# Optimization experiments

Hardware: AMD Instinct MI355X
Metric: run time of the kernel (lower is better)

The kernel has to match this reference:

```python
import jax, jax.numpy as jnp
import numpy as np

HEADS = 16
DIM_HEAD = 64
MAX_FREQ = 256.0  # lucidrains RotaryEmbedding(freqs_for='pixel', max_freq=256)


def axial_freqs(H, W, dim_head):
    # per-axis rotary dim = dim_head // 2 (RotaryEmbedding(dim=head_dim//2))
    d = dim_head // 2
    base = jnp.linspace(1.0, MAX_FREQ / 2.0, d // 2) * jnp.pi  # (d/2,)

    def axis(n):
        pos = jnp.linspace(-1.0, 1.0, n)              # pixel positions
        f = pos[:, None] * base                        # (n, d/2)
        return jnp.repeat(f, 2, axis=-1)               # (n, d) interleaved pairs

    fh = jnp.broadcast_to(axis(H)[:, None, :], (H, W, d))
    fw = jnp.broadcast_to(axis(W)[None, :, :], (H, W, d))
    return jnp.concatenate([fh, fw], axis=-1)          # (H, W, dim_head)


def apply_rope(t, freqs):
    # t: (B,T,H,W,h,d); freqs: (H,W,d)
    f = freqs[:, :, None, :]                           # broadcast over heads
    x = t.reshape(t.shape[:-1] + (t.shape[-1] // 2, 2))
    x1, x2 = x[..., 0], x[..., 1]
    rot = jnp.stack([-x2, x1], axis=-1).reshape(t.shape)  # rotate_half (interleaved)
    return t * jnp.cos(f) + rot * jnp.sin(f)


def setup_inputs() -> dict:
    key = jax.random.key(0)
    k1, k2, k3 = jax.random.split(key, 3)
    B, T, H, W, D = 1, 8, 32, 32, 1024
    inner = HEADS * DIM_HEAD
    x = jax.random.normal(k1, (B, T, H, W, D), dtype=jnp.float32)
    Wqkv = jax.random.normal(k2, (D, 3 * inner), dtype=jnp.float32) * 0.02
    Wout = jax.random.normal(k3, (inner, D), dtype=jnp.float32) * 0.02
    bout = jnp.zeros((D,), dtype=jnp.float32)
    return {"x": x, "Wqkv": Wqkv, "Wout": Wout, "bout": bout}


def reference(x, Wqkv, Wout, bout):
    B, T, H, W, D = x.shape
    qkv = x @ Wqkv                                     # (B,T,H,W,3*inner)
    q, k, v = jnp.split(qkv, 3, axis=-1)
    shp = (B, T, H, W, HEADS, DIM_HEAD)
    q, k, v = q.reshape(shp), k.reshape(shp), v.reshape(shp)
    freqs = axial_freqs(H, W, DIM_HEAD)
    q = apply_rope(q, freqs)
    k = apply_rope(k, freqs)
    S = H * W
    q = q.reshape(B * T, S, HEADS, DIM_HEAD)
    k = k.reshape(B * T, S, HEADS, DIM_HEAD)
    v = v.reshape(B * T, S, HEADS, DIM_HEAD)
    scale = 1.0 / np.sqrt(DIM_HEAD).astype(np.float32)
    att = jnp.einsum('bshd,bthd->bhst', q, k) * scale  # (BT, h, S, S)
    att = jax.nn.softmax(att, axis=-1)
    o = jnp.einsum('bhst,bthd->bshd', att, v)          # (BT, S, h, d)
    o = o.reshape(B, T, H, W, HEADS * DIM_HEAD)
    return o @ Wout + bout
```

## Files before the change

### kernel.cpp

```cpp
#include <hip/hip_runtime.h>
#include <math.h>

#define DMODEL 1024
#define NQKV   3072
#define SEQ    1024
#define NH     16
#define DH     64
#define HS     (SEQ*DH)
constexpr float PI_F   = 3.14159265358979323846f;
constexpr float LOG2E  = 1.44269504088896f;

typedef _Float16 half8   __attribute__((ext_vector_type(8)));
typedef _Float16 half4   __attribute__((ext_vector_type(4)));
typedef float    floatx4 __attribute__((ext_vector_type(4)));

__device__ __forceinline__ void gload_lds16(const _Float16* g, _Float16* l) {
    __builtin_amdgcn_global_load_lds(
        (const __attribute__((address_space(1))) unsigned int*)g,
        (__attribute__((address_space(3)))       unsigned int*)l,
        16, 0, 0);
}

__global__ __launch_bounds__(256) void cvt_f16(
    const float* __restrict__ in, _Float16* __restrict__ out, int n)
{
    int i = (blockIdx.x*256 + threadIdx.x)*8;
    if (i >= n) return;
    float4 a = *(const float4*)(in + i);
    float4 b = *(const float4*)(in + i + 4);
    half8 h;
    h[0]=(_Float16)a.x; h[1]=(_Float16)a.y; h[2]=(_Float16)a.z; h[3]=(_Float16)a.w;
    h[4]=(_Float16)b.x; h[5]=(_Float16)b.y; h[6]=(_Float16)b.z; h[7]=(_Float16)b.w;
    *(half8*)(out + i) = h;
}

__global__ __launch_bounds__(256) void tr_cvt(
    const float* __restrict__ in, _Float16* __restrict__ out, int R, int C)
{
    __shared__ float T[32][33];
    const int bx = blockIdx.x, by = blockIdx.y;
    const int tx = threadIdx.x & 31, ty = threadIdx.x >> 5;
#pragma unroll
    for (int i = 0; i < 4; ++i)
        T[ty + i*8][tx] = in[(size_t)(by*32 + ty + i*8)*C + bx*32 + tx];
    __syncthreads();
#pragma unroll
    for (int i = 0; i < 4; ++i)
        out[(size_t)(bx*32 + ty + i*8)*R + by*32 + tx] = (_Float16)T[tx][ty + i*8];
}

__global__ __launch_bounds__(256) void gemm1_f16(
    const _Float16* __restrict__ A, const _Float16* __restrict__ Bt,
    _Float16* __restrict__ C, int M, int N, int K)
{
    __shared__ _Float16 As[128*32];
    __shared__ _Float16 Bs[128*32];
    const int tid = threadIdx.x;
    const int w = tid >> 6, lane = tid & 63, quad = lane >> 4, l = lane & 15;
    const int wm = (w & 1)*64, wn = (w >> 1)*64;
    const int m0 = blockIdx.y*128, n0 = blockIdx.x*128;

    const _Float16* a0 = A  + (size_t)(m0 + w*32      + (lane>>2))*K + (lane&3)*8;
    const _Float16* a1 = A  + (size_t)(m0 + w*32 + 16 + (lane>>2))*K + (lane&3)*8;
    const _Float16* b0 = Bt + (size_t)(n0 + w*32      + (lane>>2))*K + (lane&3)*8;
    const _Float16* b1 = Bt + (size_t)(n0 + w*32 + 16 + (lane>>2))*K + (lane&3)*8;
    _Float16* lA0 = As + w*1024;
    _Float16* lA1 = As + w*1024 + 512;
    _Float16* lB0 = Bs + w*1024;
    _Float16* lB1 = Bs + w*1024 + 512;

    floatx4 acc[4][4];
#pragma unroll
    for (int i = 0; i < 4; ++i)
#pragma unroll
        for (int j = 0; j < 4; ++j)
#pragma unroll
            for (int r = 0; r < 4; ++r) acc[i][j][r] = 0.f;

    for (int k0 = 0; k0 < K; k0 += 32) {
        __syncthreads();
        gload_lds16(a0, lA0); gload_lds16(a1, lA1);
        gload_lds16(b0, lB0); gload_lds16(b1, lB1);
        a0 += 32; a1 += 32; b0 += 32; b1 += 32;
        __syncthreads();
        half8 bf[4];
#pragma unroll
        for (int nt = 0; nt < 4; ++nt)
            bf[nt] = *(half8*)&Bs[(wn + nt*16 + l)*32 + quad*8];
#pragma unroll
        for (int mt = 0; mt < 4; ++mt) {
            half8 af = *(half8*)&As[(wm + mt*16 + l)*32 + quad*8];
#pragma unroll
            for (int nt = 0; nt < 4; ++nt)
                acc[mt][nt] = __builtin_amdgcn_mfma_f32_16x16x32_f16(af, bf[nt], acc[mt][nt], 0, 0, 0);
        }
    }
#pragma unroll
    for (int mt = 0; mt < 4; ++mt)
#pragma unroll
        for (int r = 0; r < 4; ++r) {
            size_t row = m0 + wm + mt*16 + quad*4 + r;
#pragma unroll
            for (int nt = 0; nt < 4; ++nt)
                C[row*N + n0 + wn + nt*16 + l] = (_Float16)acc[mt][nt][r];
        }
}

__global__ __launch_bounds__(256) void gemm2_f16(
    const _Float16* __restrict__ A, const _Float16* __restrict__ Bt,
    const float* __restrict__ bias, float* __restrict__ C, int M, int N, int K)
{
    __shared__ _Float16 As[128*32];
    __shared__ _Float16 Bs[128*32];
    const int tid = threadIdx.x;
    const int w = tid >> 6, lane = tid & 63, quad = lane >> 4, l = lane & 15;
    const int wm = (w & 1)*64, wn = (w >> 1)*64;
    const int m0 = blockIdx.y*128, n0 = blockIdx.x*128;

    const _Float16* a0 = A  + (size_t)(m0 + w*32      + (lane>>2))*K + (lane&3)*8;
    const _Float16* a1 = A  + (size_t)(m0 + w*32 + 16 + (lane>>2))*K + (lane&3)*8;
    const _Float16* b0 = Bt + (size_t)(n0 + w*32      + (lane>>2))*K + (lane&3)*8;
    const _Float16* b1 = Bt + (size_t)(n0 + w*32 + 16 + (lane>>2))*K + (lane&3)*8;
    _Float16* lA0 = As + w*1024;
    _Float16* lA1 = As + w*1024 + 512;
    _Float16* lB0 = Bs + w*1024;
    _Float16* lB1 = Bs + w*1024 + 512;

    floatx4 acc[4][4];
#pragma unroll
    for (int i = 0; i < 4; ++i)
#pragma unroll
        for (int j = 0; j < 4; ++j)
#pragma unroll
            for (int r = 0; r < 4; ++r) acc[i][j][r] = 0.f;

    for (int k0 = 0; k0 < K; k0 += 32) {
        __syncthreads();
        gload_lds16(a0, lA0); gload_lds16(a1, lA1);
        gload_lds16(b0, lB0); gload_lds16(b1, lB1);
        a0 += 32; a1 += 32; b0 += 32; b1 += 32;
        __syncthreads();
        half8 bf[4];
#pragma unroll
        for (int nt = 0; nt < 4; ++nt)
            bf[nt] = *(half8*)&Bs[(wn + nt*16 + l)*32 + quad*8];
#pragma unroll
        for (int mt = 0; mt < 4; ++mt) {
            half8 af = *(half8*)&As[(wm + mt*16 + l)*32 + quad*8];
#pragma unroll
            for (int nt = 0; nt < 4; ++nt)
                acc[mt][nt] = __builtin_amdgcn_mfma_f32_16x16x32_f16(af, bf[nt], acc[mt][nt], 0, 0, 0);
        }
    }
#pragma unroll
    for (int mt = 0; mt < 4; ++mt)
#pragma unroll
        for (int r = 0; r < 4; ++r) {
            size_t row = m0 + wm + mt*16 + quad*4 + r;
#pragma unroll
            for (int nt = 0; nt < 4; ++nt) {
                int col = n0 + wn + nt*16 + l;
                C[row*N + col] = acc[mt][nt][r] + bias[col];
            }
        }
}

__global__ __launch_bounds__(256) void rope_scatter(
    const _Float16* __restrict__ qkv,
    _Float16* __restrict__ qw, _Float16* __restrict__ kw,
    _Float16* __restrict__ vt)
{
    const int sc = blockIdx.x;
    const int bh = blockIdx.y;
    const int bt = bh >> 4, head = bh & 15;
    const int s0 = sc*64;
    const int tid = threadIdx.x;
    const int d0 = (tid & 7)*8;

    __shared__ _Float16 T[64][80];

#pragma unroll
    for (int half = 0; half < 2; ++half) {
        const int r = (tid >> 3) + half*32;
        const int s = s0 + r;
        const _Float16* src = qkv + (size_t)(bt*SEQ + s)*NQKV + head*DH + d0;
        half8 hq = *(const half8*)(src);
        half8 hk = *(const half8*)(src + DMODEL);
        half8 hv = *(const half8*)(src + 2*DMODEL);
        float fq[8], fk[8];
#pragma unroll
        for (int j = 0; j < 8; ++j) { fq[j] = (float)hq[j]; fk[j] = (float)hk[j]; }
        const int hp = s >> 5, wp = s & 31;
        const float ph = -1.0f + hp*(2.0f/31.0f);
        const float pw = -1.0f + wp*(2.0f/31.0f);
#pragma unroll
        for (int p = 0; p < 4; ++p) {
            int pg = (d0 >> 1) + p;
            float pos = (pg < 16) ? ph : pw;
            int   gi  = (pg < 16) ? pg : (pg - 16);
            float th  = pos * ((1.0f + gi*(127.0f/15.0f)) * PI_F);
            float sn, cs;
            sincosf(th, &sn, &cs);
            float q1 = fq[2*p], q2 = fq[2*p+1];
            fq[2*p]   = q1*cs - q2*sn;
            fq[2*p+1] = q2*cs + q1*sn;
            float k1 = fk[2*p], k2 = fk[2*p+1];
            fk[2*p]   = k1*cs - k2*sn;
            fk[2*p+1] = k2*cs + k1*sn;
        }
        half8 oq, ok;
        const float qsc = 0.125f * LOG2E;
#pragma unroll
        for (int j = 0; j < 8; ++j) {
            oq[j] = (_Float16)(fq[j]*qsc);
            ok[j] = (_Float16)fk[j];
        }
        *(half8*)(qw + (size_t)bh*HS + (size_t)s*DH + d0) = oq;
        *(half8*)(kw + (size_t)bh*HS + (size_t)s*DH + d0) = ok;
#pragma unroll
        for (int j = 0; j < 8; ++j) T[d0 + j][r] = hv[j];
    }
    __syncthreads();
    const int d = tid >> 2, so = (tid & 3)*16;
    half8 v0 = *(half8*)&T[d][so];
    half8 v1 = *(half8*)&T[d][so + 8];
    _Float16* dst = vt + (size_t)bh*HS + (size_t)d*SEQ + s0 + so;
    *(half8*)dst       = v0;
    *(half8*)(dst + 8) = v1;
}

#define BC  64
#define LDH 72

__global__ __launch_bounds__(256) void attn_mfma(
    const _Float16* __restrict__ qw, const _Float16* __restrict__ kw,
    const _Float16* __restrict__ vt, _Float16* __restrict__ om)
{
    const int qc = blockIdx.x;
    const int bh = blockIdx.y;
    const int tid  = threadIdx.x;
    const int w    = tid >> 6;
    const int lane = tid & 63;
    const int quad = lane >> 4;
    const int l    = lane & 15;

    __shared__ _Float16 Ks[2][BC][LDH];
    __shared__ _Float16 Vs[2][DH][LDH];
    __shared__ _Float16 Ps[4][16][LDH];
    __shared__ float    Ls[4][16];

    const _Float16* qp = qw + (size_t)bh*HS + (size_t)(qc*64 + w*16)*DH;
    const _Float16* kp = kw + (size_t)bh*HS;
    const _Float16* vp = vt + (size_t)bh*HS;

    half8 qf0 = *(const half8*)(qp + (size_t)l*DH + quad*8);
    half8 qf1 = *(const half8*)(qp + (size_t)l*DH + quad*8 + 32);

    const int rs = tid >> 3;
    const int cs = (tid & 7)*8;

    half8 kr0 = *(const half8*)(kp + (size_t)rs*DH + cs);
    half8 kr1 = *(const half8*)(kp + (size_t)(rs+32)*DH + cs);
    half8 vr0 = *(const half8*)(vp + (size_t)rs*SEQ + cs);
    half8 vr1 = *(const half8*)(vp + (size_t)(rs+32)*SEQ + cs);
    *(half8*)&Ks[0][rs][cs]    = kr0;
    *(half8*)&Ks[0][rs+32][cs] = kr1;
    *(half8*)&Vs[0][rs][cs]    = vr0;
    *(half8*)&Vs[0][rs+32][cs] = vr1;

    floatx4 Of[4];
#pragma unroll
    for (int dt = 0; dt < 4; ++dt)
#pragma unroll
        for (int r = 0; r < 4; ++r) Of[dt][r] = 0.f;
    float lsum = 0.f;

    __syncthreads();

    for (int kc = 0; kc < SEQ/BC; ++kc) {
        const int cur = kc & 1;
        if (kc < SEQ/BC - 1) {
            const _Float16* kn = kp + (size_t)(kc+1)*BC*DH;
            const _Float16* vn = vp + (size_t)(kc+1)*BC;
            kr0 = *(const half8*)(kn + (size_t)rs*DH + cs);
            kr1 = *(const half8*)(kn + (size_t)(rs+32)*DH + cs);
            vr0 = *(const half8*)(vn + (size_t)rs*SEQ + cs);
            vr1 = *(const half8*)(vn + (size_t)(rs+32)*SEQ + cs);
        }

        floatx4 Sf[4];
#pragma unroll
        for (int kg = 0; kg < 4; ++kg) {
            half8 af0 = *(half8*)&Ks[cur][kg*16 + l][quad*8];
            half8 af1 = *(half8*)&Ks[cur][kg*16 + l][quad*8 + 32];
            floatx4 a;
#pragma unroll
            for (int r = 0; r < 4; ++r) a[r] = 0.f;
            a = __builtin_amdgcn_mfma_f32_16x16x32_f16(af0, qf0, a, 0, 0, 0);
            a = __builtin_amdgcn_mfma_f32_16x16x32_f16(af1, qf1, a, 0, 0, 0);
            Sf[kg] = a;
        }
#pragma unroll
        for (int kg = 0; kg < 4; ++kg) {
            half4 p4;
#pragma unroll
            for (int r = 0; r < 4; ++r) {
                float p = __builtin_amdgcn_exp2f(Sf[kg][r]);
                lsum += p;
                p4[r] = (_Float16)p;
            }
            *(half4*)&Ps[w][l][kg*16 + quad*4] = p4;
        }
        half8 pa0 = *(half8*)&Ps[w][l][quad*8];
        half8 pa1 = *(half8*)&Ps[w][l][quad*8 + 32];
#pragma unroll
        for (int dt = 0; dt < 4; ++dt) {
            half8 vb0 = *(half8*)&Vs[cur][dt*16 + l][quad*8];
            half8 vb1 = *(half8*)&Vs[cur][dt*16 + l][quad*8 + 32];
            Of[dt] = __builtin_amdgcn_mfma_f32_16x16x32_f16(pa0, vb0, Of[dt], 0, 0, 0);
            Of[dt] = __builtin_amdgcn_mfma_f32_16x16x32_f16(pa1, vb1, Of[dt], 0, 0, 0);
        }

        if (kc < SEQ/BC - 1) {
            *(half8*)&Ks[1-cur][rs][cs]    = kr0;
            *(half8*)&Ks[1-cur][rs+32][cs] = kr1;
            *(half8*)&Vs[1-cur][rs][cs]    = vr0;
            *(half8*)&Vs[1-cur][rs+32][cs] = vr1;
        }
        __syncthreads();
    }

    lsum += __shfl_xor(lsum, 16);
    lsum += __shfl_xor(lsum, 32);
    if (quad == 0) Ls[w][l] = lsum;
    float inv[4];
#pragma unroll
    for (int r = 0; r < 4; ++r) inv[r] = 1.0f / Ls[w][quad*4 + r];

    const int bt = bh >> 4, head = bh & 15;
    _Float16* opf = om + (size_t)(bt*SEQ + qc*64 + w*16)*DMODEL + head*DH;
#pragma unroll
    for (int dt = 0; dt < 4; ++dt)
#pragma unroll
        for (int r = 0; r < 4; ++r)
            opf[(size_t)(quad*4 + r)*DMODEL + dt*16 + l] =
                (_Float16)(Of[dt][r]*inv[r]);
}

extern "C" void kernel_launch(void* const* d_in, const int* in_sizes, int n_in,
                              void* d_out, int out_size, void* d_ws, size_t ws_size,
                              hipStream_t stream)
{
    const float* x    = (const float*)d_in[0];
    const float* Wqkv = (const float*)d_in[1];
    const float* Wout = (const float*)d_in[2];
    const float* bout = (const float*)d_in[3];
    float* out = (float*)d_out;

    _Float16* ws   = (_Float16*)d_ws;
    _Float16* Xh   = ws;
    _Float16* Wqkt = ws + 8388608;
    _Float16* Wot  = ws + 11534336;
    _Float16* qkvt = ws + 12582912;
    _Float16* qw   = ws + 37748736;
    _Float16* kw   = ws + 46137344;
    _Float16* vt   = ws + 54525952;
    _Float16* om   = qkvt;

    hipLaunchKernelGGL(cvt_f16, dim3(4096), dim3(256), 0, stream,
                       x, Xh, 8388608);
    hipLaunchKernelGGL(tr_cvt, dim3(96, 32), dim3(256), 0, stream,
                       Wqkv, Wqkt, 1024, 3072);
    hipLaunchKernelGGL(tr_cvt, dim3(32, 32), dim3(256), 0, stream,
                       Wout, Wot, 1024, 1024);
    hipLaunchKernelGGL(gemm1_f16, dim3(24, 64), dim3(256), 0, stream,
                       Xh, Wqkt, qkvt, 8192, NQKV, DMODEL);
    hipLaunchKernelGGL(rope_scatter, dim3(16, 128), dim3(256), 0, stream,
                       qkvt, qw, kw, vt);
    hipLaunchKernelGGL(attn_mfma, dim3(16, 128), dim3(256), 0, stream,
                       qw, kw, vt, om);
    hipLaunchKernelGGL(gemm2_f16, dim3(8, 64), dim3(256), 0, stream,
                       om, Wot, bout, out, 8192, DMODEL, DMODEL);
}
```

Baseline: 278.4 us.

## Process 32 query rows per wave in attention to reuse K/V tiles

Each wave in the attention kernel now handles two 16-row query tiles instead of one, so a block covers 128 queries and the grid along the query axis is halved. Every K and V tile loaded into LDS feeds twice as many MFMA operations, which halves global K/V traffic and LDS staging per query. The LDS row padding also changes from 72 to 68 halves to alter the bank-conflict pattern. The cost is higher register pressure and fewer blocks. A 136-byte row stride also breaks 16-byte alignment for the half8 LDS accesses.

Measured after the change: 270.8 us. 1.03x faster.

```diff
diff --git a/kernel.cpp b/kernel.cpp
--- a/kernel.cpp
+++ b/kernel.cpp
@@ -230,7 +230,7 @@
 }
 
 #define BC  64
-#define LDH 72
+#define LDH 68
 
 __global__ __launch_bounds__(256) void attn_mfma(
     const _Float16* __restrict__ qw, const _Float16* __restrict__ kw,
@@ -246,15 +246,19 @@
 
     __shared__ _Float16 Ks[2][BC][LDH];
     __shared__ _Float16 Vs[2][DH][LDH];
-    __shared__ _Float16 Ps[4][16][LDH];
-    __shared__ float    Ls[4][16];
-
-    const _Float16* qp = qw + (size_t)bh*HS + (size_t)(qc*64 + w*16)*DH;
+    __shared__ _Float16 Ps[4][32][LDH];
+    __shared__ float    Ls[4][32];
+
+    const _Float16* qp = qw + (size_t)bh*HS + (size_t)(qc*128 + w*32)*DH;
     const _Float16* kp = kw + (size_t)bh*HS;
     const _Float16* vp = vt + (size_t)bh*HS;
 
-    half8 qf0 = *(const half8*)(qp + (size_t)l*DH + quad*8);
-    half8 qf1 = *(const half8*)(qp + (size_t)l*DH + quad*8 + 32);
+    half8 qf[2][2];
+#pragma unroll
+    for (int qt = 0; qt < 2; ++qt) {
+        qf[qt][0] = *(const half8*)(qp + (size_t)(qt*16 + l)*DH + quad*8);
+        qf[qt][1] = *(const half8*)(qp + (size_t)(qt*16 + l)*DH + quad*8 + 32);
+    }
 
     const int rs = tid >> 3;
     const int cs = (tid & 7)*8;
@@ -268,12 +272,14 @@
     *(half8*)&Vs[0][rs][cs]    = vr0;
     *(half8*)&Vs[0][rs+32][cs] = vr1;
 
-    floatx4 Of[4];
-#pragma unroll
-    for (int dt = 0; dt < 4; ++dt)
-#pragma unroll
-        for (int r = 0; r < 4; ++r) Of[dt][r] = 0.f;
-    float lsum = 0.f;
+    floatx4 Of[2][4];
+#pragma unroll
+    for (int qt = 0; qt < 2; ++qt)
+#pragma unroll
+        for (int dt = 0; dt < 4; ++dt)
+#pragma unroll
+            for (int r = 0; r < 4; ++r) Of[qt][dt][r] = 0.f;
+    float lsum[2] = {0.f, 0.f};
 
     __syncthreads();
 
@@ -288,37 +294,49 @@
             vr1 = *(const half8*)(vn + (size_t)(rs+32)*SEQ + cs);
         }
 
-        floatx4 Sf[4];
+        floatx4 Sf[2][4];
 #pragma unroll
         for (int kg = 0; kg < 4; ++kg) {
             half8 af0 = *(half8*)&Ks[cur][kg*16 + l][quad*8];
             half8 af1 = *(half8*)&Ks[cur][kg*16 + l][quad*8 + 32];
-            floatx4 a;
-#pragma unroll
-            for (int r = 0; r < 4; ++r) a[r] = 0.f;
-            a = __builtin_amdgcn_mfma_f32_16x16x32_f16(af0, qf0, a, 0, 0, 0);
-            a = __builtin_amdgcn_mfma_f32_16x16x32_f16(af1, qf1, a, 0, 0, 0);
-            Sf[kg] = a;
-        }
-#pragma unroll
-        for (int kg = 0; kg < 4; ++kg) {
-            half4 p4;
-#pragma unroll
-            for (int r = 0; r < 4; ++r) {
-                float p = __builtin_amdgcn_exp2f(Sf[kg][r]);
-                lsum += p;
-                p4[r] = (_Float16)p;
+#pragma unroll
+            for (int qt = 0; qt < 2; ++qt) {
+                floatx4 a;
+#pragma unroll
+                for (int r = 0; r < 4; ++r) a[r] = 0.f;
+                a = __builtin_amdgcn_mfma_f32_16x16x32_f16(af0, qf[qt][0], a, 0, 0, 0);
+                a = __builtin_amdgcn_mfma_f32_16x16x32_f16(af1, qf[qt][1], a, 0, 0, 0);
+                Sf[qt][kg] = a;
             }
-            *(half4*)&Ps[w][l][kg*16 + quad*4] = p4;
-        }
-        half8 pa0 = *(half8*)&Ps[w][l][quad*8];
-        half8 pa1 = *(half8*)&Ps[w][l][quad*8 + 32];
+        }
+#pragma unroll
+        for (int qt = 0; qt < 2; ++qt)
+#pragma unroll
+            for (int kg = 0; kg < 4; ++kg) {
+                half4 p4;
+#pragma unroll
+                for (int r = 0; r < 4; ++r) {
+                    float p = __builtin_amdgcn_exp2f(Sf[qt][kg][r]);
+                    lsum[qt] += p;
+                    p4[r] = (_Float16)p;
+                }
+                *(half4*)&Ps[w][qt*16 + l][kg*16 + quad*4] = p4;
+            }
+        half8 pa[2][2];
+#pragma unroll
+        for (int qt = 0; qt < 2; ++qt) {
+            pa[qt][0] = *(half8*)&Ps[w][qt*16 + l][quad*8];
+            pa[qt][1] = *(half8*)&Ps[w][qt*16 + l][quad*8 + 32];
+        }
 #pragma unroll
         for (int dt = 0; dt < 4; ++dt) {
             half8 vb0 = *(half8*)&Vs[cur][dt*16 + l][quad*8];
             half8 vb1 = *(half8*)&Vs[cur][dt*16 + l][quad*8 + 32];
-            Of[dt] = __builtin_amdgcn_mfma_f32_16x16x32_f16(pa0, vb0, Of[dt], 0, 0, 0);
-            Of[dt] = __builtin_amdgcn_mfma_f32_16x16x32_f16(pa1, vb1, Of[dt], 0, 0, 0);
+#pragma unroll
+            for (int qt = 0; qt < 2; ++qt) {
+                Of[qt][dt] = __builtin_amdgcn_mfma_f32_16x16x32_f16(pa[qt][0], vb0, Of[qt][dt], 0, 0, 0);
+                Of[qt][dt] = __builtin_amdgcn_mfma_f32_16x16x32_f16(pa[qt][1], vb1, Of[qt][dt], 0, 0, 0);
+            }
         }
 
         if (kc < SEQ/BC - 1) {
@@ -330,21 +348,26 @@
         __syncthreads();
     }
 
-    lsum += __shfl_xor(lsum, 16);
-    lsum += __shfl_xor(lsum, 32);
-    if (quad == 0) Ls[w][l] = lsum;
-    float inv[4];
-#pragma unroll
-    for (int r = 0; r < 4; ++r) inv[r] = 1.0f / Ls[w][quad*4 + r];
-
+#pragma unroll
+    for (int qt = 0; qt < 2; ++qt) {
+        lsum[qt] += __shfl_xor(lsum[qt], 16);
+        lsum[qt] += __shfl_xor(lsum[qt], 32);
+        if (quad == 0) Ls[w][qt*16 + l] = lsum[qt];
+    }
     const int bt = bh >> 4, head = bh & 15;
-    _Float16* opf = om + (size_t)(bt*SEQ + qc*64 + w*16)*DMODEL + head*DH;
-#pragma unroll
-    for (int dt = 0; dt < 4; ++dt)
-#pragma unroll
-        for (int r = 0; r < 4; ++r)
-            opf[(size_t)(quad*4 + r)*DMODEL + dt*16 + l] =
-                (_Float16)(Of[dt][r]*inv[r]);
+    _Float16* opf = om + (size_t)(bt*SEQ + qc*128 + w*32)*DMODEL + head*DH;
+#pragma unroll
+    for (int qt = 0; qt < 2; ++qt) {
+        float inv[4];
+#pragma unroll
+        for (int r = 0; r < 4; ++r) inv[r] = 1.0f / Ls[w][qt*16 + quad*4 + r];
+#pragma unroll
+        for (int dt = 0; dt < 4; ++dt)
+#pragma unroll
+            for (int r = 0; r < 4; ++r)
+                opf[(size_t)(qt*16 + quad*4 + r)*DMODEL + dt*16 + l] =
+                    (_Float16)(Of[qt][dt][r]*inv[r]);
+    }
 }
 
 extern "C" void kernel_launch(void* const* d_in, const int* in_sizes, int n_in,
@@ -377,7 +400,7 @@
                        Xh, Wqkt, qkvt, 8192, NQKV, DMODEL);
     hipLaunchKernelGGL(rope_scatter, dim3(16, 128), dim3(256), 0, stream,
                        qkvt, qw, kw, vt);
-    hipLaunchKernelGGL(attn_mfma, dim3(16, 128), dim3(256), 0, stream,
+    hipLaunchKernelGGL(attn_mfma, dim3(8, 128), dim3(256), 0, stream,
                        qw, kw, vt, om);
     hipLaunchKernelGGL(gemm2_f16, dim3(8, 64), dim3(256), 0, stream,
                        om, Wot, bout, out, 8192, DMODEL, DMODEL);
```
